# Kernel optimization log

Hardware: AMD Instinct MI355X
Metric: run time of the kernel (lower is better)

Reference implementation:

```python
import jax, jax.numpy as jnp
import numpy as np

N = 50000      # nodes
E = 800000     # edges (before self loops)
IN = 128       # in_dim
HID = 16       # hidden_dim per head
HEADS = 8
OUT = 64       # out_dim
NEG_SLOPE = 0.2  # PyG GATConv default leaky_relu slope


def add_self_loops(edge_index, n):
    loops = jnp.arange(n, dtype=edge_index.dtype)
    return jnp.concatenate([edge_index, jnp.stack([loops, loops])], axis=1)


def gat_layer(x, edge_index, W, att_src, att_dst, bias, concat):
    # x: [N, F_in], W: [F_in, H*C], att_*: [H, C], bias: [H*C] or [C]
    H, C = att_src.shape
    n = x.shape[0]
    h = (x @ W).reshape(n, H, C)                     # [N,H,C]
    a_src = jnp.sum(h * att_src, axis=-1)            # [N,H]
    a_dst = jnp.sum(h * att_dst, axis=-1)            # [N,H]
    src, dst = edge_index[0], edge_index[1]
    e = jax.nn.leaky_relu(a_src[src] + a_dst[dst], NEG_SLOPE)   # [E,H]
    # segment softmax over incoming edges of each destination node
    m = jax.ops.segment_max(e, dst, num_segments=n)             # [N,H]
    e = jnp.exp(e - m[dst])
    s = jax.ops.segment_sum(e, dst, num_segments=n)             # [N,H]
    alpha = e / (s[dst] + 1e-16)                                # [E,H]
    msg = h[src] * alpha[:, :, None]                            # [E,H,C]
    out = jax.ops.segment_sum(msg, dst, num_segments=n)         # [N,H,C]
    out = out.reshape(n, H * C) if concat else out.mean(axis=1)
    return out + bias


def setup_inputs() -> dict:
    key = jax.random.key(0)
    ks = jax.random.split(key, 10)
    x = jax.random.normal(ks[0], (N, IN), dtype=jnp.float32)
    edge_index = jax.random.randint(ks[1], (2, E), 0, N, dtype=jnp.int32)
    sc = 0.1
    W1 = jax.random.normal(ks[2], (IN, HEADS * HID), jnp.float32) * sc
    att_src1 = jax.random.normal(ks[3], (HEADS, HID), jnp.float32) * sc
    att_dst1 = jax.random.normal(ks[4], (HEADS, HID), jnp.float32) * sc
    b1 = jnp.zeros((HEADS * HID,), jnp.float32)
    W2 = jax.random.normal(ks[5], (HEADS * HID, OUT), jnp.float32) * sc
    att_src2 = jax.random.normal(ks[6], (1, OUT), jnp.float32) * sc
    att_dst2 = jax.random.normal(ks[7], (1, OUT), jnp.float32) * sc
    b2 = jnp.zeros((OUT,), jnp.float32)
    return {"x": x, "edge_index": edge_index,
            "W1": W1, "att_src1": att_src1, "att_dst1": att_dst1, "b1": b1,
            "W2": W2, "att_src2": att_src2, "att_dst2": att_dst2, "b2": b2}


def reference(x, edge_index, W1, att_src1, att_dst1, b1, W2, att_src2, att_dst2, b2):
    ei = add_self_loops(edge_index, x.shape[0])
    h = gat_layer(x, ei, W1, att_src1, att_dst1, b1, concat=True)   # [N, HEADS*HID]
    h = jax.nn.elu(h)
    out = gat_layer(h, ei, W2, att_src2, att_dst2, b2, concat=False)  # [N, OUT]
    return out
```

## Files before the change

### kernel.cpp

```cpp
#include <hip/hip_runtime.h>
#include <hip/hip_bf16.h>

#define HEADS 8
#define HID 16
#define F1 128
#define OUTD 64
#define BWL 7
#define BW 128
#define MAXBUK 512
#define BCAP 3584
#define CHUNK 2048

typedef unsigned int uint;
typedef unsigned short ushort;
typedef __attribute__((ext_vector_type(8))) short bfrag;
typedef __attribute__((ext_vector_type(4))) float f32x4;

__device__ __forceinline__ ushort f2bf(float f) {
  __hip_bfloat16 b = __float2bfloat16(f);
  return *reinterpret_cast<ushort*>(&b);
}
__device__ __forceinline__ float bf2f_lo(uint w) {
  return __uint_as_float((w & 0xFFFFu) << 16);
}
__device__ __forceinline__ float bf2f_hi(uint w) {
  return __uint_as_float(w & 0xFFFF0000u);
}
__device__ __forceinline__ uint elu2(uint u) {
  float lo = bf2f_lo(u), hi = bf2f_hi(u);
  lo = lo > 0.f ? lo : __expf(lo) - 1.f;
  hi = hi > 0.f ? hi : __expf(hi) - 1.f;
  return (uint)f2bf(lo) | ((uint)f2bf(hi) << 16);
}

__global__ void k_wcvt(const float* __restrict__ W1, const float* __restrict__ W2,
                       ushort* __restrict__ W1t, ushort* __restrict__ W2t,
                       int* __restrict__ bukcur, int NBUK) {
  int o = blockIdx.x * 256 + threadIdx.x;
  if (o < F1 * F1) {
    int c = o >> 7, k = o & 127;
    W1t[o] = f2bf(W1[k * F1 + c]);
  } else if (o < F1 * F1 + OUTD * F1) {
    int i = o - F1 * F1;
    int c = i >> 7, k = i & 127;
    W2t[i] = f2bf(W2[k * OUTD + c]);
  } else {
    int i = o - (F1 * F1 + OUTD * F1);
    if (i < NBUK) bukcur[i] = 0;
  }
}


__global__ __launch_bounds__(256) void k_scatter(const int* __restrict__ ei, int E, int N,
                                                 int* __restrict__ bukcur,
                                                 int* __restrict__ pairs) {
  __shared__ int hist[MAXBUK];
  int t = threadIdx.x;
  hist[t] = 0; hist[t + 256] = 0;
  __syncthreads();
  long long e0 = (long long)blockIdx.x * CHUNK;
  int ET = E + N;
  int myP[8], myB[8];
#pragma unroll
  for (int i = 0; i < 8; ++i) {
    long long e = e0 + i * 256 + t;
    if (e < ET) {
      int s = e < E ? ei[e] : (int)(e - E);
      int d = e < E ? ei[E + e] : (int)(e - E);
      myP[i] = s | ((d & (BW - 1)) << 20);
      myB[i] = d >> BWL;
      atomicAdd(&hist[myB[i]], 1);
    } else {
      myB[i] = -1;
    }
  }
  __syncthreads();
  for (int b = t; b < MAXBUK; b += 256) {
    int c = hist[b];
    hist[b] = c ? (b * BCAP + atomicAdd(&bukcur[b], c)) : 0;
  }
  __syncthreads();
#pragma unroll
  for (int i = 0; i < 8; ++i) {
    if (myB[i] >= 0) {
      int pos = atomicAdd(&hist[myB[i]], 1);
      pairs[pos] = myP[i];
    }
  }
}

__global__ __launch_bounds__(256) void k_csr(const int* __restrict__ pairs,
                                             const int* __restrict__ bukcur,
                                             int* __restrict__ off, int* __restrict__ offe,
                                             int* __restrict__ csr, int N) {
  __shared__ int cnt[BW];
  __shared__ int cur[BW];
  int b = blockIdx.x, t = threadIdx.x;
  int beg = b * BCAP, end = beg + bukcur[b];
  if (t < BW) cnt[t] = 0;
  __syncthreads();
  for (int j = beg + t; j < end; j += 256)
    atomicAdd(&cnt[(pairs[j] >> 20) & (BW - 1)], 1);
  __syncthreads();
  int my = t < BW ? cnt[t] : 0;
  for (int o = 1; o < BW; o <<= 1) {
    int v = (t < BW && t >= o) ? cnt[t - o] : 0;
    __syncthreads();
    if (t < BW) cnt[t] += v;
    __syncthreads();
  }
  if (t < BW) {
    int start = beg + cnt[t] - my;
    cur[t] = start;
    int d0 = b * BW + t;
    if (d0 < N) { off[d0] = start; offe[d0] = start + my; }
  }
  __syncthreads();
  for (int j = beg + t; j < end; j += 256) {
    int pr = pairs[j];
    int pos = atomicAdd(&cur[(pr >> 20) & (BW - 1)], 1);
    csr[pos] = pr & 0xFFFFF;
  }
}

__global__ __launch_bounds__(256) void k_gemm1(
    const float* __restrict__ x, const ushort* __restrict__ W1t,
    const float* __restrict__ as, const float* __restrict__ ad,
    uint* __restrict__ hA, uint* __restrict__ hB,
    float* __restrict__ a_src, float* __restrict__ a_dst, int N) {
  __shared__ __align__(16) ushort xl[64 * 136];
  __shared__ __align__(16) ushort wl[128 * 136];
  int tx = threadIdx.x;
  int r0 = blockIdx.x * 64;

  {
    int c = tx >> 1, k0 = (tx & 1) * 64;
    const uint4* g = reinterpret_cast<const uint4*>(W1t + c * F1 + k0);
#pragma unroll
    for (int j = 0; j < 8; ++j)
      *reinterpret_cast<uint4*>(&wl[c * 136 + k0 + j * 8]) = g[j];
  }
  {
    int row = tx & 63, kq = tx >> 6;
    bool act = (r0 + row) < N;
    const float4* xg = reinterpret_cast<const float4*>(x + (size_t)(r0 + row) * F1 + kq * 32);
#pragma unroll
    for (int j = 0; j < 4; ++j) {
      float4 va = act ? xg[2 * j]     : make_float4(0.f, 0.f, 0.f, 0.f);
      float4 vb = act ? xg[2 * j + 1] : make_float4(0.f, 0.f, 0.f, 0.f);
      uint4 pk;
      pk.x = (uint)f2bf(va.x) | ((uint)f2bf(va.y) << 16);
      pk.y = (uint)f2bf(va.z) | ((uint)f2bf(va.w) << 16);
      pk.z = (uint)f2bf(vb.x) | ((uint)f2bf(vb.y) << 16);
      pk.w = (uint)f2bf(vb.z) | ((uint)f2bf(vb.w) << 16);
      *reinterpret_cast<uint4*>(&xl[row * 136 + kq * 32 + j * 8]) = pk;
    }
  }
  __syncthreads();

  int w = tx >> 6, l = tx & 63;
  int lr = l & 15, lo = l >> 4;

  bfrag af[4];
#pragma unroll
  for (int ks = 0; ks < 4; ++ks)
    af[ks] = *reinterpret_cast<const bfrag*>(&xl[(w * 16 + lr) * 136 + ks * 32 + lo * 8]);

  f32x4 acc[8];
#pragma unroll
  for (int n0 = 0; n0 < 8; ++n0) {
    acc[n0] = (f32x4){0.f, 0.f, 0.f, 0.f};
#pragma unroll
    for (int ks = 0; ks < 4; ++ks) {
      bfrag bf = *reinterpret_cast<const bfrag*>(&wl[(n0 * 16 + lr) * 136 + ks * 32 + lo * 8]);
      acc[n0] = __builtin_amdgcn_mfma_f32_16x16x32_bf16(af[ks], bf, acc[n0], 0, 0, 0);
    }
  }

#pragma unroll
  for (int n0 = 0; n0 < 8; ++n0) {
    float asv = as[n0 * 16 + lr];
    float adv = ad[n0 * 16 + lr];
    ushort* tp = reinterpret_cast<ushort*>(n0 < 4 ? hA : hB);
    int cbase = (n0 & 3) * 16 + lr;
#pragma unroll
    for (int r = 0; r < 4; ++r) {
      int row = r0 + w * 16 + lo * 4 + r;
      float hv = acc[n0][r];
      float ps = hv * asv, pd = hv * adv;
      ps += __shfl_xor(ps, 1); ps += __shfl_xor(ps, 2);
      ps += __shfl_xor(ps, 4); ps += __shfl_xor(ps, 8);
      pd += __shfl_xor(pd, 1); pd += __shfl_xor(pd, 2);
      pd += __shfl_xor(pd, 4); pd += __shfl_xor(pd, 8);
      if (row < N) {
        tp[(size_t)row * 64 + cbase] = f2bf(hv);
        if (lr == 0) {
          a_src[row * HEADS + n0] = ps;
          a_dst[row * HEADS + n0] = pd;
        }
      }
    }
  }
}

__global__ void k_agg1h(const int* __restrict__ off, const int* __restrict__ offe,
                        const int* __restrict__ csr,
                        const uint2* __restrict__ htab, const float* __restrict__ a_src,
                        const float* __restrict__ a_dst, const float* __restrict__ b1,
                        uint* __restrict__ out1b, int N, int hbase, int obase) {
  int w = threadIdx.x >> 6, lane = threadIdx.x & 63;
  int q = lane >> 4, c2 = lane & 15;
  int h = hbase + (c2 >> 2);
  int d = blockIdx.x * 4 + w;
  if (d >= N) return;
  int beg = off[d], end = offe[d];
  float adl = a_dst[d * HEADS + h];
  float a0 = 0.f, a1 = 0.f, a2 = 0.f, a3 = 0.f, den = 0.f;
#pragma unroll 2
  for (int j = beg + q; j < end; j += 4) {
    int s = csr[j];
    float v = a_src[s * HEADS + h] + adl;
    v = v >= 0.f ? v : 0.2f * v;
    float p = __expf(v);
    uint2 wd = htab[(size_t)s * 16 + c2];
    a0 = fmaf(p, bf2f_lo(wd.x), a0);
    a1 = fmaf(p, bf2f_hi(wd.x), a1);
    a2 = fmaf(p, bf2f_lo(wd.y), a2);
    a3 = fmaf(p, bf2f_hi(wd.y), a3);
    den += p;
  }
  a0 += __shfl_xor(a0, 16); a0 += __shfl_xor(a0, 32);
  a1 += __shfl_xor(a1, 16); a1 += __shfl_xor(a1, 32);
  a2 += __shfl_xor(a2, 16); a2 += __shfl_xor(a2, 32);
  a3 += __shfl_xor(a3, 16); a3 += __shfl_xor(a3, 32);
  den += __shfl_xor(den, 16); den += __shfl_xor(den, 32);
  if (q == 0) {
    float inv = 1.f / den;
    float4 bb = *reinterpret_cast<const float4*>(&b1[obase + 4 * c2]);
    uint2 o;
    o.x = (uint)f2bf(a0 * inv + bb.x) | ((uint)f2bf(a1 * inv + bb.y) << 16);
    o.y = (uint)f2bf(a2 * inv + bb.z) | ((uint)f2bf(a3 * inv + bb.w) << 16);
    *reinterpret_cast<uint2*>(&out1b[(size_t)d * 64 + (obase >> 1) + 2 * c2]) = o;
  }
}

__global__ __launch_bounds__(256) void k_gemm2(
    const uint* __restrict__ out1b, const ushort* __restrict__ W2t,
    const float* __restrict__ as2, const float* __restrict__ ad2,
    uint* __restrict__ h2b, float* __restrict__ a_src2,
    float* __restrict__ a_dst2, int N) {
  __shared__ __align__(16) ushort xl[64 * 136];
  __shared__ __align__(16) ushort wl[64 * 136];
  int tx = threadIdx.x;
  int r0 = blockIdx.x * 64;

  {
    int c = tx & 63, k0 = (tx >> 6) * 32;
    const uint4* g = reinterpret_cast<const uint4*>(W2t + c * F1 + k0);
#pragma unroll
    for (int j = 0; j < 4; ++j)
      *reinterpret_cast<uint4*>(&wl[c * 136 + k0 + j * 8]) = g[j];
  }
  {
    int row = tx & 63, kq = tx >> 6;
    bool act = (r0 + row) < N;
    const uint4* xg = reinterpret_cast<const uint4*>(out1b + (size_t)(r0 + row) * 64 + kq * 16);
#pragma unroll
    for (int j = 0; j < 4; ++j) {
      uint4 v = act ? xg[j] : make_uint4(0, 0, 0, 0);
      uint4 pk;
      pk.x = elu2(v.x);
      pk.y = elu2(v.y);
      pk.z = elu2(v.z);
      pk.w = elu2(v.w);
      *reinterpret_cast<uint4*>(&xl[row * 136 + kq * 32 + j * 8]) = pk;
    }
  }
  __syncthreads();

  int w = tx >> 6, l = tx & 63;
  int lr = l & 15, lo = l >> 4;

  bfrag af[4];
#pragma unroll
  for (int ks = 0; ks < 4; ++ks)
    af[ks] = *reinterpret_cast<const bfrag*>(&xl[(w * 16 + lr) * 136 + ks * 32 + lo * 8]);

  f32x4 acc[4];
#pragma unroll
  for (int n0 = 0; n0 < 4; ++n0) {
    acc[n0] = (f32x4){0.f, 0.f, 0.f, 0.f};
#pragma unroll
    for (int ks = 0; ks < 4; ++ks) {
      bfrag bf = *reinterpret_cast<const bfrag*>(&wl[(n0 * 16 + lr) * 136 + ks * 32 + lo * 8]);
      acc[n0] = __builtin_amdgcn_mfma_f32_16x16x32_bf16(af[ks], bf, acc[n0], 0, 0, 0);
    }
  }

  float asv[4], adv[4];
#pragma unroll
  for (int n0 = 0; n0 < 4; ++n0) {
    asv[n0] = as2[n0 * 16 + lr];
    adv[n0] = ad2[n0 * 16 + lr];
  }
  ushort* tp = reinterpret_cast<ushort*>(h2b);
#pragma unroll
  for (int r = 0; r < 4; ++r) {
    int row = r0 + w * 16 + lo * 4 + r;
    float ps = 0.f, pd = 0.f;
#pragma unroll
    for (int n0 = 0; n0 < 4; ++n0) {
      float hv = acc[n0][r];
      ps = fmaf(hv, asv[n0], ps);
      pd = fmaf(hv, adv[n0], pd);
    }
    ps += __shfl_xor(ps, 1); ps += __shfl_xor(ps, 2);
    ps += __shfl_xor(ps, 4); ps += __shfl_xor(ps, 8);
    pd += __shfl_xor(pd, 1); pd += __shfl_xor(pd, 2);
    pd += __shfl_xor(pd, 4); pd += __shfl_xor(pd, 8);
    if (row < N) {
#pragma unroll
      for (int n0 = 0; n0 < 4; ++n0)
        tp[(size_t)row * 64 + n0 * 16 + lr] = f2bf(acc[n0][r]);
      if (lr == 0) {
        a_src2[row] = ps;
        a_dst2[row] = pd;
      }
    }
  }
}

__global__ void k_agg2(const int* __restrict__ off, const int* __restrict__ offe,
                       const int* __restrict__ csr,
                       const uint4* __restrict__ h2b4, const float* __restrict__ a_src2,
                       const float* __restrict__ a_dst2, const float* __restrict__ b2,
                       float* __restrict__ out, int N) {
  int w = threadIdx.x >> 6, lane = threadIdx.x & 63;
  int g = lane >> 3, c4 = lane & 7;
  int d = blockIdx.x * 4 + w;
  if (d >= N) return;
  int beg = off[d], end = offe[d];
  float adl = a_dst2[d];
  float a[8] = {0.f, 0.f, 0.f, 0.f, 0.f, 0.f, 0.f, 0.f};
  float den = 0.f;
  for (int j = beg + g; j < end; j += 8) {
    int s = csr[j];
    float v = a_src2[s] + adl;
    v = v >= 0.f ? v : 0.2f * v;
    float p = __expf(v);
    uint4 wd = h2b4[(size_t)s * 8 + c4];
    a[0] = fmaf(p, bf2f_lo(wd.x), a[0]);
    a[1] = fmaf(p, bf2f_hi(wd.x), a[1]);
    a[2] = fmaf(p, bf2f_lo(wd.y), a[2]);
    a[3] = fmaf(p, bf2f_hi(wd.y), a[3]);
    a[4] = fmaf(p, bf2f_lo(wd.z), a[4]);
    a[5] = fmaf(p, bf2f_hi(wd.z), a[5]);
    a[6] = fmaf(p, bf2f_lo(wd.w), a[6]);
    a[7] = fmaf(p, bf2f_hi(wd.w), a[7]);
    den += p;
  }
#pragma unroll
  for (int i = 0; i < 8; ++i) {
    a[i] += __shfl_xor(a[i], 8);
    a[i] += __shfl_xor(a[i], 16);
    a[i] += __shfl_xor(a[i], 32);
  }
  den += __shfl_xor(den, 8); den += __shfl_xor(den, 16); den += __shfl_xor(den, 32);
  if (g == 0) {
    float inv = 1.f / den;
    float4 b0 = *reinterpret_cast<const float4*>(&b2[8 * c4]);
    float4 b1v = *reinterpret_cast<const float4*>(&b2[8 * c4 + 4]);
    float4 o0, o1;
    o0.x = a[0] * inv + b0.x;  o0.y = a[1] * inv + b0.y;
    o0.z = a[2] * inv + b0.z;  o0.w = a[3] * inv + b0.w;
    o1.x = a[4] * inv + b1v.x; o1.y = a[5] * inv + b1v.y;
    o1.z = a[6] * inv + b1v.z; o1.w = a[7] * inv + b1v.w;
    *reinterpret_cast<float4*>(&out[(size_t)d * OUTD + 8 * c4]) = o0;
    *reinterpret_cast<float4*>(&out[(size_t)d * OUTD + 8 * c4 + 4]) = o1;
  }
}

extern "C" void kernel_launch(void* const* d_in, const int* in_sizes, int n_in,
                              void* d_out, int out_size, void* d_ws, size_t ws_size,
                              hipStream_t stream) {
  const float* x   = (const float*)d_in[0];
  const int*   ei  = (const int*)d_in[1];
  const float* W1  = (const float*)d_in[2];
  const float* as1 = (const float*)d_in[3];
  const float* ad1 = (const float*)d_in[4];
  const float* b1  = (const float*)d_in[5];
  const float* W2  = (const float*)d_in[6];
  const float* as2 = (const float*)d_in[7];
  const float* ad2 = (const float*)d_in[8];
  const float* b2  = (const float*)d_in[9];
  float* out = (float*)d_out;

  int N = in_sizes[0] / F1;
  int E = in_sizes[1] / 2;
  int ET = E + N;
  int NBUK = (N + BW - 1) / BW;
  int NCH = (ET + CHUNK - 1) / CHUNK;
  int NT = (N + 63) / 64;
  int NWC = (F1 * F1 + OUTD * F1 + MAXBUK + 255) / 256;

  char* p = (char*)d_ws;
  auto alloc = [&](size_t bytes) {
    char* q = p;
    p += (bytes + 15) & ~(size_t)15;
    return q;
  };
  int* bukcur  = (int*)alloc((size_t)NBUK * 4);
  int* off     = (int*)alloc((size_t)N * 4);
  int* offe    = (int*)alloc((size_t)N * 4);
  int* pairs   = (int*)alloc((size_t)NBUK * BCAP * 4);
  int* csr     = (int*)alloc((size_t)NBUK * BCAP * 4);
  ushort* W1t  = (ushort*)alloc((size_t)F1 * F1 * 2);
  ushort* W2t  = (ushort*)alloc((size_t)OUTD * F1 * 2);
  uint* hA     = (uint*)alloc((size_t)N * 32 * 4);
  uint* hB     = (uint*)alloc((size_t)N * 32 * 4);
  uint* h2b    = (uint*)alloc((size_t)N * 32 * 4);
  uint* out1b  = (uint*)alloc((size_t)N * 64 * 4);
  float* a_src1 = (float*)alloc((size_t)N * HEADS * 4);
  float* a_dst1 = (float*)alloc((size_t)N * HEADS * 4);
  float* a_src2 = (float*)alloc((size_t)N * 4);
  float* a_dst2 = (float*)alloc((size_t)N * 4);

  hipLaunchKernelGGL(k_wcvt, dim3(NWC), dim3(256), 0, stream, W1, W2, W1t, W2t, bukcur, NBUK);
  hipLaunchKernelGGL(k_scatter, dim3(NCH), dim3(256), 0, stream, ei, E, N, bukcur, pairs);
  hipLaunchKernelGGL(k_csr, dim3(NBUK), dim3(256), 0, stream,
                     pairs, bukcur, off, offe, csr, N);

  hipLaunchKernelGGL(k_gemm1, dim3(NT), dim3(256), 0, stream,
                     x, W1t, as1, ad1, hA, hB, a_src1, a_dst1, N);
  hipLaunchKernelGGL(k_agg1h, dim3((N + 3) / 4), dim3(256), 0, stream,
                     off, offe, csr, (const uint2*)hA, a_src1, a_dst1, b1, out1b, N, 0, 0);
  hipLaunchKernelGGL(k_agg1h, dim3((N + 3) / 4), dim3(256), 0, stream,
                     off, offe, csr, (const uint2*)hB, a_src1, a_dst1, b1, out1b, N, 4, 64);

  hipLaunchKernelGGL(k_gemm2, dim3(NT), dim3(256), 0, stream,
                     out1b, W2t, as2, ad2, h2b, a_src2, a_dst2, N);
  hipLaunchKernelGGL(k_agg2, dim3((N + 3) / 4), dim3(256), 0, stream,
                     off, offe, csr, (const uint4*)h2b, a_src2, a_dst2, b2, out, N);
}
```

Before: 164.1 us.

## Merge edge scatter and first GEMM into one launch; widen CSR build blocks

Folds the edge bucket-scatter kernel and the first-layer projection GEMM into one kernel, with blocks dispatched by block index and one shared-memory buffer reused by both roles. The two independent stages can then run concurrently on the GPU and one launch boundary goes away. The CSR build kernel also moves to 512 threads per block. The fused kernel takes the larger shared-memory footprint for every block, which can lower occupancy for the scatter blocks.

```diff
diff --git a/kernel.cpp b/kernel.cpp
--- a/kernel.cpp
+++ b/kernel.cpp
@@ -50,88 +50,55 @@
   }
 }
 
-
-__global__ __launch_bounds__(256) void k_scatter(const int* __restrict__ ei, int E, int N,
-                                                 int* __restrict__ bukcur,
-                                                 int* __restrict__ pairs) {
-  __shared__ int hist[MAXBUK];
-  int t = threadIdx.x;
-  hist[t] = 0; hist[t + 256] = 0;
-  __syncthreads();
-  long long e0 = (long long)blockIdx.x * CHUNK;
-  int ET = E + N;
-  int myP[8], myB[8];
-#pragma unroll
-  for (int i = 0; i < 8; ++i) {
-    long long e = e0 + i * 256 + t;
-    if (e < ET) {
-      int s = e < E ? ei[e] : (int)(e - E);
-      int d = e < E ? ei[E + e] : (int)(e - E);
-      myP[i] = s | ((d & (BW - 1)) << 20);
-      myB[i] = d >> BWL;
-      atomicAdd(&hist[myB[i]], 1);
-    } else {
-      myB[i] = -1;
-    }
-  }
-  __syncthreads();
-  for (int b = t; b < MAXBUK; b += 256) {
-    int c = hist[b];
-    hist[b] = c ? (b * BCAP + atomicAdd(&bukcur[b], c)) : 0;
-  }
-  __syncthreads();
-#pragma unroll
-  for (int i = 0; i < 8; ++i) {
-    if (myB[i] >= 0) {
-      int pos = atomicAdd(&hist[myB[i]], 1);
-      pairs[pos] = myP[i];
-    }
-  }
-}
-
-__global__ __launch_bounds__(256) void k_csr(const int* __restrict__ pairs,
-                                             const int* __restrict__ bukcur,
-                                             int* __restrict__ off, int* __restrict__ offe,
-                                             int* __restrict__ csr, int N) {
-  __shared__ int cnt[BW];
-  __shared__ int cur[BW];
-  int b = blockIdx.x, t = threadIdx.x;
-  int beg = b * BCAP, end = beg + bukcur[b];
-  if (t < BW) cnt[t] = 0;
-  __syncthreads();
-  for (int j = beg + t; j < end; j += 256)
-    atomicAdd(&cnt[(pairs[j] >> 20) & (BW - 1)], 1);
-  __syncthreads();
-  int my = t < BW ? cnt[t] : 0;
-  for (int o = 1; o < BW; o <<= 1) {
-    int v = (t < BW && t >= o) ? cnt[t - o] : 0;
-    __syncthreads();
-    if (t < BW) cnt[t] += v;
-    __syncthreads();
-  }
-  if (t < BW) {
-    int start = beg + cnt[t] - my;
-    cur[t] = start;
-    int d0 = b * BW + t;
-    if (d0 < N) { off[d0] = start; offe[d0] = start + my; }
-  }
-  __syncthreads();
-  for (int j = beg + t; j < end; j += 256) {
-    int pr = pairs[j];
-    int pos = atomicAdd(&cur[(pr >> 20) & (BW - 1)], 1);
-    csr[pos] = pr & 0xFFFFF;
-  }
-}
-
-__global__ __launch_bounds__(256) void k_gemm1(
+__global__ __launch_bounds__(256) void k_sg(
+    const int* __restrict__ ei, int E, int N, int* __restrict__ bukcur,
+    int* __restrict__ pairs,
     const float* __restrict__ x, const ushort* __restrict__ W1t,
     const float* __restrict__ as, const float* __restrict__ ad,
     uint* __restrict__ hA, uint* __restrict__ hB,
-    float* __restrict__ a_src, float* __restrict__ a_dst, int N) {
-  __shared__ __align__(16) ushort xl[64 * 136];
-  __shared__ __align__(16) ushort wl[128 * 136];
+    float* __restrict__ a_src, float* __restrict__ a_dst, int NCH_) {
+  __shared__ __align__(16) char smem[52224];
   int tx = threadIdx.x;
-  int r0 = blockIdx.x * 64;
+
+  if ((int)blockIdx.x < NCH_) {
+    int* hist = (int*)smem;
+    hist[tx] = 0; hist[tx + 256] = 0;
+    __syncthreads();
+    long long e0 = (long long)blockIdx.x * CHUNK;
+    int ET = E + N;
+    int myP[8], myB[8];
+#pragma unroll
+    for (int i = 0; i < 8; ++i) {
+      long long e = e0 + i * 256 + tx;
+      if (e < ET) {
+        int s = e < E ? ei[e] : (int)(e - E);
+        int d = e < E ? ei[E + e] : (int)(e - E);
+        myP[i] = s | ((d & (BW - 1)) << 20);
+        myB[i] = d >> BWL;
+        atomicAdd(&hist[myB[i]], 1);
+      } else {
+        myB[i] = -1;
+      }
+    }
+    __syncthreads();
+    for (int b = tx; b < MAXBUK; b += 256) {
+      int c = hist[b];
+      hist[b] = c ? (b * BCAP + atomicAdd(&bukcur[b], c)) : 0;
+    }
+    __syncthreads();
+#pragma unroll
+    for (int i = 0; i < 8; ++i) {
+      if (myB[i] >= 0) {
+        int pos = atomicAdd(&hist[myB[i]], 1);
+        pairs[pos] = myP[i];
+      }
+    }
+    return;
+  }
+
+  ushort* xl = (ushort*)smem;
+  ushort* wl = xl + 64 * 136;
+  int r0 = ((int)blockIdx.x - NCH_) * 64;
 
   {
     int c = tx >> 1, k0 = (tx & 1) * 64;
@@ -200,6 +167,40 @@
         }
       }
     }
+  }
+}
+
+__global__ __launch_bounds__(512) void k_csr(const int* __restrict__ pairs,
+                                             const int* __restrict__ bukcur,
+                                             int* __restrict__ off, int* __restrict__ offe,
+                                             int* __restrict__ csr, int N) {
+  __shared__ int cnt[BW];
+  __shared__ int cur[BW];
+  int b = blockIdx.x, t = threadIdx.x;
+  int beg = b * BCAP, end = beg + bukcur[b];
+  if (t < BW) cnt[t] = 0;
+  __syncthreads();
+  for (int j = beg + t; j < end; j += 512)
+    atomicAdd(&cnt[(pairs[j] >> 20) & (BW - 1)], 1);
+  __syncthreads();
+  int my = t < BW ? cnt[t] : 0;
+  for (int o = 1; o < BW; o <<= 1) {
+    int v = (t < BW && t >= o) ? cnt[t - o] : 0;
+    __syncthreads();
+    if (t < BW) cnt[t] += v;
+    __syncthreads();
+  }
+  if (t < BW) {
+    int start = beg + cnt[t] - my;
+    cur[t] = start;
+    int d0 = b * BW + t;
+    if (d0 < N) { off[d0] = start; offe[d0] = start + my; }
+  }
+  __syncthreads();
+  for (int j = beg + t; j < end; j += 512) {
+    int pr = pairs[j];
+    int pos = atomicAdd(&cur[(pr >> 20) & (BW - 1)], 1);
+    csr[pos] = pr & 0xFFFFF;
   }
 }
 
@@ -426,12 +427,12 @@
   float* a_dst2 = (float*)alloc((size_t)N * 4);
 
   hipLaunchKernelGGL(k_wcvt, dim3(NWC), dim3(256), 0, stream, W1, W2, W1t, W2t, bukcur, NBUK);
-  hipLaunchKernelGGL(k_scatter, dim3(NCH), dim3(256), 0, stream, ei, E, N, bukcur, pairs);
-  hipLaunchKernelGGL(k_csr, dim3(NBUK), dim3(256), 0, stream,
+  hipLaunchKernelGGL(k_sg, dim3(NCH + NT), dim3(256), 0, stream,
+                     ei, E, N, bukcur, pairs,
+                     x, W1t, as1, ad1, hA, hB, a_src1, a_dst1, NCH);
+  hipLaunchKernelGGL(k_csr, dim3(NBUK), dim3(512), 0, stream,
                      pairs, bukcur, off, offe, csr, N);
 
-  hipLaunchKernelGGL(k_gemm1, dim3(NT), dim3(256), 0, stream,
-                     x, W1t, as1, ad1, hA, hB, a_src1, a_dst1, N);
   hipLaunchKernelGGL(k_agg1h, dim3((N + 3) / 4), dim3(256), 0, stream,
                      off, offe, csr, (const uint2*)hA, a_src1, a_dst1, b1, out1b, N, 0, 0);
   hipLaunchKernelGGL(k_agg1h, dim3((N + 3) / 4), dim3(256), 0, stream,
```

After: 154.5 us. 1.06x faster.
